# Optimization experiments

Measured on AMD Instinct MI355X. Metric: run time of the kernel, lower is better.

Reference implementation:

```python
import jax, jax.numpy as jnp
import numpy as np

B, U, V = 4, 64, 256
IN_DIM, STATE_DIM, CODE_DIM = 768, 768, 384
NUM_HEADS, HEAD_DIM = 8, 64
INNER = NUM_HEADS * HEAD_DIM  # 512
SCALE = HEAD_DIM ** 0.5


def _ln(x, g, b, eps=1e-5):
    mu = jnp.mean(x, axis=-1, keepdims=True)
    var = jnp.var(x, axis=-1, keepdims=True)
    return (x - mu) * jax.lax.rsqrt(var + eps) * g + b


def setup_inputs() -> dict:
    key = jax.random.key(0)
    ks = jax.random.split(key, 12)
    def w(k, shape, s=0.02):
        return jax.random.normal(k, shape, jnp.float32) * s
    return {
        "receiver_states": jax.random.normal(ks[0], (B, U, STATE_DIM), jnp.float32),
        "receiver_codes": jax.random.normal(ks[1], (B, U, CODE_DIM), jnp.float32),
        "sender_states": jax.random.normal(ks[2], (B, V, IN_DIM), jnp.float32),
        "ln_r_g": jnp.ones((STATE_DIM,), jnp.float32),
        "ln_r_b": jnp.zeros((STATE_DIM,), jnp.float32),
        "ln_s_g": jnp.ones((IN_DIM,), jnp.float32),
        "ln_s_b": jnp.zeros((IN_DIM,), jnp.float32),
        "Wq": w(ks[3], (STATE_DIM, INNER)), "bq": jnp.zeros((INNER,), jnp.float32), "Wmq": w(ks[4], (CODE_DIM, STATE_DIM)),
        "Wk": w(ks[5], (IN_DIM, INNER)),   "bk": jnp.zeros((INNER,), jnp.float32), "Wmk": w(ks[6], (CODE_DIM, IN_DIM)),
        "Wv": w(ks[7], (IN_DIM, INNER)),   "bv": jnp.zeros((INNER,), jnp.float32), "Wmv": w(ks[8], (CODE_DIM, IN_DIM)),
        "We": w(ks[9], (INNER, STATE_DIM)), "be": jnp.zeros((STATE_DIM,), jnp.float32), "Wme": w(ks[10], (CODE_DIM, INNER)),
        "gamma": jnp.ones((STATE_DIM,), jnp.float32),  # LayerScale, init 1.0
    }


def reference(receiver_states, receiver_codes, sender_states,
              ln_r_g, ln_r_b, ln_s_g, ln_s_b,
              Wq, bq, Wmq, Wk, bk, Wmk, Wv, bv, Wmv, We, be, Wme, gamma):
    r = _ln(receiver_states, ln_r_g, ln_r_b)   # (b,u,ds)
    s = _ln(sender_states, ln_s_g, ln_s_b)     # (b,v,di)
    # ModFC: y = (x * (1 + ctx @ Wm)) @ W + b  (code-conditioned input modulation)
    q = (r * (1.0 + receiver_codes @ Wmq)) @ Wq + bq          # (b,u,inner)
    mk = 1.0 + receiver_codes @ Wmk                           # (b,u,di)
    mv = 1.0 + receiver_codes @ Wmv                           # (b,u,di)
    xs = s[:, :, None, :]                                     # (b,v,1,di)
    k = (xs * mk[:, None, :, :]) @ Wk + bk                    # (b,v,u,inner)
    v = (xs * mv[:, None, :, :]) @ Wv + bv                    # (b,v,u,inner)
    qh = q.reshape(B, U, NUM_HEADS, HEAD_DIM)
    kh = k.reshape(B, V, U, NUM_HEADS, HEAD_DIM)
    vh = v.reshape(B, V, U, NUM_HEADS, HEAD_DIM)
    scores = jnp.einsum('buhc,bvuhc->bhuv', qh, kh) / SCALE   # (b,h,u,v)
    weights = jax.nn.softmax(scores, axis=-1)
    msg = jnp.einsum('bhuv,bvuhc->buhc', weights, vh).reshape(B, U, INNER)
    out = (msg * (1.0 + receiver_codes @ Wme)) @ We + be      # exit ModFC -> (b,u,ds)
    out = out * gamma                                         # LayerScale
    return receiver_states + out                              # residual
```

## Files before the change

kernel.cpp:

```cpp
#include <hip/hip_runtime.h>


#define DD 768
#define CDIM 384
#define NH 8
#define HD 64
#define INNER 512
#define VV 256

__device__ __forceinline__ void fma4(float4& a, float s, const float4& b) {
  a.x += s * b.x; a.y += s * b.y; a.z += s * b.z; a.w += s * b.w;
}

__device__ __forceinline__ void fma_chunk8(const float* __restrict__ Aw,
                                           int lda, int kk, const float4* b,
                                           float4* acc) {
#pragma unroll
  for (int rg = 0; rg < 4; rg++) {
    const float* ap = Aw + (rg * 2) * lda + kk;
    float4 a0l = *(const float4*)(ap);
    float4 a0h = *(const float4*)(ap + 4);
    float4 a1l = *(const float4*)(ap + lda);
    float4 a1h = *(const float4*)(ap + lda + 4);
    float4* ac = acc + rg * 2;
    fma4(ac[0], a0l.x, b[0]); fma4(ac[1], a1l.x, b[0]);
    fma4(ac[0], a0l.y, b[1]); fma4(ac[1], a1l.y, b[1]);
    fma4(ac[0], a0l.z, b[2]); fma4(ac[1], a1l.z, b[2]);
    fma4(ac[0], a0l.w, b[3]); fma4(ac[1], a1l.w, b[3]);
    fma4(ac[0], a0h.x, b[4]); fma4(ac[1], a1h.x, b[4]);
    fma4(ac[0], a0h.y, b[5]); fma4(ac[1], a1h.y, b[5]);
    fma4(ac[0], a0h.z, b[6]); fma4(ac[1], a1h.z, b[6]);
    fma4(ac[0], a0h.w, b[7]); fma4(ac[1], a1h.w, b[7]);
  }
}

template <int KQ, int NS>
__device__ __forceinline__ void gcore8(const float* __restrict__ Aw, int lda,
                                       const float* __restrict__ Bp,
                                       float4* acc) {
  float4 b0[8], b1[8];
  const float* Bq = Bp;
#pragma unroll
  for (int i = 0; i < 8; i++) b0[i] = *(const float4*)(Bq + (size_t)i * NS);
  Bq += (size_t)8 * NS;
#pragma unroll 1
  for (int kk = 0; kk + 16 <= KQ; kk += 16) {
#pragma unroll
    for (int i = 0; i < 8; i++) b1[i] = *(const float4*)(Bq + (size_t)i * NS);
    Bq += (size_t)8 * NS;
    fma_chunk8(Aw, lda, kk, b0, acc);
    if (kk + 16 < KQ) {
#pragma unroll
      for (int i = 0; i < 8; i++) b0[i] = *(const float4*)(Bq + (size_t)i * NS);
      Bq += (size_t)8 * NS;
    }
    fma_chunk8(Aw, lda, kk + 8, b1, acc);
  }
}

__device__ __forceinline__ void kred(float4* acc, float* RED, int wid,
                                     int kl) {
  __syncthreads();
  float4* R4 = (float4*)RED;
  int rg = wid & 1, kh = wid >> 1;
  if (kh) {
#pragma unroll
    for (int r = 0; r < 8; r++) R4[(rg * 8 + r) * 64 + kl] = acc[r];
  }
  __syncthreads();
  if (!kh) {
#pragma unroll
    for (int r = 0; r < 8; r++) {
      float4 v = R4[(rg * 8 + r) * 64 + kl];
      acc[r].x += v.x; acc[r].y += v.y; acc[r].z += v.z; acc[r].w += v.w;
    }
  }
}

__global__ __launch_bounds__(256, 2) void k_s1(
    const float* __restrict__ ss, const float* __restrict__ rs,
    const float* __restrict__ g_s, const float* __restrict__ b_s,
    const float* __restrict__ g_r, const float* __restrict__ b_r,
    const float* __restrict__ codes, const float* __restrict__ Wmq,
    const float* __restrict__ Wmk, const float* __restrict__ Wmv,
    const float* __restrict__ Wme, const float* __restrict__ Wk,
    float* __restrict__ s_ln, float* __restrict__ r_ln,
    float* __restrict__ cp, float* __restrict__ WkT) {
  __shared__ __align__(16) float SB[6144];
  int bid = blockIdx.x, t = threadIdx.x;
  if (bid < 176) {
    int nc = bid % 11, mb = bid / 11;
    int base = nc * 256;
    const float* W; int N, colW;
    if (base < 768)       { W = Wmq; N = DD;    colW = base; }
    else if (base < 1536) { W = Wmk; N = DD;    colW = base - 768; }
    else if (base < 2304) { W = Wmv; N = DD;    colW = base - 1536; }
    else                  { W = Wme; N = INNER; colW = base - 2304; }
    int m0 = mb * 16;
#pragma unroll
    for (int p = 0; p < 24; p++) {
      int idx = p * 256 + t, r = idx / 384, k = idx % 384;
      SB[idx] = codes[(size_t)(m0 + r) * CDIM + k];
    }
    __syncthreads();
    int kl = t & 63, wid = t >> 6, rg = wid & 1, kh = wid >> 1;
    float4 acc[8] = {};
    const float* Aw = SB + (rg * 8) * 384 + kh * 192;
    if (N == DD)
      gcore8<192, DD>(Aw, 384, W + (size_t)(kh * 192) * DD + colW + 4 * kl, acc);
    else
      gcore8<192, INNER>(Aw, 384, W + (size_t)(kh * 192) * INNER + colW + 4 * kl, acc);
    kred(acc, SB, wid, kl);
    if (!kh) {
      int gcol = base + 4 * kl;
#pragma unroll
      for (int j = 0; j < 8; j++)
        *(float4*)(cp + (size_t)(m0 + rg * 8 + j) * 2816 + gcol) = acc[j];
    }
  } else if (bid < 272) {
    int tid = bid - 176;
    int d0 = (tid >> 3) * 64, c0 = (tid & 7) * 64;
    int j = t & 63, i0 = t >> 6;
#pragma unroll
    for (int p = 0; p < 16; p++) {
      int i = p * 4 + i0;
      SB[i * 65 + j] = Wk[(size_t)(d0 + i) * INNER + c0 + j];
    }
    __syncthreads();
#pragma unroll
    for (int p = 0; p < 16; p++) {
      int i = p * 4 + i0;
      WkT[(size_t)(c0 + i) * DD + d0 + j] = SB[j * 65 + i];
    }
  } else {
    int rr = bid - 272;
    const float *x, *g, *bb; float* y; int r;
    if (rr < 1024) { x = ss; g = g_s; bb = b_s; y = s_ln; r = rr; }
    else           { x = rs; g = g_r; bb = b_r; y = r_ln; r = rr - 1024; }
    const float* xr = x + (size_t)r * DD;
    float v0 = xr[t], v1 = xr[t + 256], v2 = xr[t + 512];
    float s = v0 + v1 + v2, sq = v0 * v0 + v1 * v1 + v2 * v2;
    for (int o = 32; o > 0; o >>= 1) {
      s += __shfl_down(s, o, 64); sq += __shfl_down(sq, o, 64);
    }
    int wid = t >> 6, lane = t & 63;
    if (lane == 0) { SB[wid] = s; SB[wid + 4] = sq; }
    __syncthreads();
    float sum = SB[0] + SB[1] + SB[2] + SB[3];
    float ssq = SB[4] + SB[5] + SB[6] + SB[7];
    float mu = sum * (1.0f / 768.0f);
    float var = ssq * (1.0f / 768.0f) - mu * mu;
    float rstd = rsqrtf(var + 1e-5f);
    float* yr = y + (size_t)r * DD;
    yr[t]       = (v0 - mu) * rstd * g[t]       + bb[t];
    yr[t + 256] = (v1 - mu) * rstd * g[t + 256] + bb[t + 256];
    yr[t + 512] = (v2 - mu) * rstd * g[t + 512] + bb[t + 512];
  }
}

__global__ __launch_bounds__(256, 2) void k_s2(
    const float* __restrict__ s_ln, const float* __restrict__ r_ln,
    const float* __restrict__ cp, const float* __restrict__ Wq,
    float* __restrict__ sT, float* __restrict__ qp) {
  __shared__ __align__(16) float SB[4160];
  int bid = blockIdx.x, t = threadIdx.x;
  if (bid < 128) {
    int ks = bid & 3, tile = bid >> 2, nc = tile & 1, mb = tile >> 1;
    int m0 = mb * 16, col0 = nc * 256, k0 = ks * 192;
#pragma unroll
    for (int p = 0; p < 12; p++) {
      int idx = p * 256 + t, r = idx / 192, k = idx % 192;
      int d = k0 + k;
      float mqv = cp[(size_t)(m0 + r) * 2816 + d] + 1.0f;
      SB[idx] = r_ln[(size_t)(m0 + r) * DD + d] * mqv;
    }
    __syncthreads();
    int kl = t & 63, wid = t >> 6, rg = wid & 1, kh = wid >> 1;
    int col = col0 + 4 * kl;
    float4 acc[8] = {};
    gcore8<96, INNER>(SB + (rg * 8) * 192 + kh * 96, 192,
                      Wq + (size_t)(k0 + kh * 96) * INNER + col, acc);
    kred(acc, SB, wid, kl);
    if (!kh) {
      float* dst = qp + (size_t)ks * (256 * INNER);
#pragma unroll
      for (int j = 0; j < 8; j++)
        *(float4*)(dst + (size_t)(m0 + rg * 8 + j) * INNER + col) = acc[j];
    }
  } else {
    int tid = bid - 128;
    int vt = tid & 3, dt = (tid >> 2) % 12, b = tid / 48;
    int v0 = vt * 64, d0 = dt * 64;
    int j = t & 63, i0 = t >> 6;
#pragma unroll
    for (int p = 0; p < 16; p++) {
      int i = p * 4 + i0;
      SB[i * 65 + j] = s_ln[(size_t)(b * VV + v0 + i) * DD + d0 + j];
    }
    __syncthreads();
#pragma unroll
    for (int p = 0; p < 16; p++) {
      int i = p * 4 + i0;
      sT[((size_t)b * DD + d0 + i) * VV + v0 + j] = SB[j * 65 + i];
    }
  }
}

__global__ __launch_bounds__(256, 2) void k_s3(
    const float* __restrict__ qp, const float* __restrict__ bq,
    const float* __restrict__ WkT, const float* __restrict__ cp,
    const float* __restrict__ bk, float* __restrict__ qm,
    float* __restrict__ qbk) {
  __shared__ __align__(16) float SB[4096];
  int bid = blockIdx.x, t = threadIdx.x;
  if (bid < 384) {
    int h = bid & 7, dc = (bid >> 3) % 3, mb = bid / 24;
    int m0 = mb * 16;
#pragma unroll
    for (int p = 0; p < 4; p++) {
      int idx = p * 256 + t, r = idx >> 6, c = idx & 63;
      int i = h * HD + c;
      size_t off = (size_t)(m0 + r) * INNER + i;
      SB[idx] = qp[off] + qp[131072 + off] + qp[262144 + off] +
                qp[393216 + off] + bq[i];
    }
    __syncthreads();
    int kl = t & 63, wid = t >> 6, rg = wid & 1, kh = wid >> 1;
    int col = dc * 256 + 4 * kl;
    float4 acc[8] = {};
    gcore8<32, DD>(SB + (rg * 8) * HD + kh * 32, HD,
                   WkT + (size_t)(h * HD + kh * 32) * DD + col, acc);
    kred(acc, SB, wid, kl);
    if (!kh) {
#pragma unroll
      for (int j = 0; j < 8; j++) {
        int m = m0 + rg * 8 + j;
        const float* mkp = cp + (size_t)m * 2816 + 768 + col;
        float4 o = {acc[j].x * (mkp[0] + 1.0f), acc[j].y * (mkp[1] + 1.0f),
                    acc[j].z * (mkp[2] + 1.0f), acc[j].w * (mkp[3] + 1.0f)};
        *(float4*)(qm + ((size_t)m * NH + h) * DD + col) = o;
      }
    }
  } else {
    int m = bid - 384;
    size_t off = (size_t)m * INNER;
    SB[t] = (qp[off + t] + qp[131072 + off + t] + qp[262144 + off + t] +
             qp[393216 + off + t] + bq[t]) * bk[t];
    int t2 = t + 256;
    SB[t2] = (qp[off + t2] + qp[131072 + off + t2] + qp[262144 + off + t2] +
              qp[393216 + off + t2] + bq[t2]) * bk[t2];
    __syncthreads();
    if (t < 8) {
      float a = 0.f;
      for (int c = 0; c < HD; c++) a += SB[t * HD + c];
      qbk[m * NH + t] = a;
    }
  }
}

__global__ __launch_bounds__(256, 2) void k_s4(
    const float* __restrict__ qm, const float* __restrict__ sT,
    float* __restrict__ scp) {
  __shared__ __align__(16) float SB[4096];
  int bid = blockIdx.x, t = threadIdx.x;
  int ks = bid & 3, b = (bid >> 2) & 3, mb = bid >> 4;
  int gi0 = b * 512 + mb * 16, k0 = ks * 192;
#pragma unroll
  for (int p = 0; p < 12; p++) {
    int idx = p * 256 + t, r = idx / 192, k = idx % 192;
    SB[idx] = qm[(size_t)(gi0 + r) * DD + k0 + k];
  }
  __syncthreads();
  int kl = t & 63, wid = t >> 6, rg = wid & 1, kh = wid >> 1;
  int col = 4 * kl;
  float4 acc[8] = {};
  gcore8<96, VV>(SB + (rg * 8) * 192 + kh * 96, 192,
                 sT + ((size_t)b * DD + k0 + kh * 96) * VV + col, acc);
  kred(acc, SB, wid, kl);
  if (!kh) {
    float* dst = scp + (size_t)ks * (2048 * VV);
#pragma unroll
    for (int j = 0; j < 8; j++)
      *(float4*)(dst + (size_t)(gi0 + rg * 8 + j) * VV + col) = acc[j];
  }
}

__global__ __launch_bounds__(256, 2) void k_s5(
    const float* __restrict__ scp, const float* __restrict__ qbk,
    const float* __restrict__ s_ln, const float* __restrict__ cp,
    float* __restrict__ wsm) {
  __shared__ __align__(16) float SC[4096];
  int bid = blockIdx.x, t = threadIdx.x;
  int dc = bid % 3, up = (bid / 3) % 32, b = bid / 96;
  int gi0 = b * 512 + up * 16;
#pragma unroll
  for (int p = 0; p < 16; p++) {
    int idx = p * 256 + t, r = idx >> 8, c = idx & 255;
    size_t o = (size_t)(gi0 + r) * VV + c;
    float v = scp[o] + scp[524288 + o] + scp[1048576 + o] + scp[1572864 + o];
    int m = b * 64 + up * 2 + (r >> 3), h = r & 7;
    SC[idx] = (v + qbk[m * NH + h]) * 0.125f;
  }
  __syncthreads();
  int wid = t >> 6, lane = t & 63;
#pragma unroll
  for (int j = 0; j < 4; j++) {
    int r = wid * 4 + j;
    float x0 = SC[r * 256 + lane],       x1 = SC[r * 256 + lane + 64];
    float x2 = SC[r * 256 + lane + 128], x3 = SC[r * 256 + lane + 192];
    float mx = fmaxf(fmaxf(x0, x1), fmaxf(x2, x3));
    for (int o = 1; o < 64; o <<= 1) mx = fmaxf(mx, __shfl_xor(mx, o, 64));
    float e0 = __expf(x0 - mx), e1 = __expf(x1 - mx);
    float e2 = __expf(x2 - mx), e3 = __expf(x3 - mx);
    float sm = e0 + e1 + e2 + e3;
    for (int o = 1; o < 64; o <<= 1) sm += __shfl_xor(sm, o, 64);
    float rinv = 1.0f / sm;
    SC[r * 256 + lane] = e0 * rinv;       SC[r * 256 + lane + 64] = e1 * rinv;
    SC[r * 256 + lane + 128] = e2 * rinv; SC[r * 256 + lane + 192] = e3 * rinv;
  }
  __syncthreads();
  int kl = t & 63, rg = wid & 1, kh = wid >> 1;
  int col = dc * 256 + 4 * kl;
  float4 acc[8] = {};
  gcore8<128, DD>(SC + (rg * 8) * 256 + kh * 128, 256,
                  s_ln + (size_t)(b * VV + kh * 128) * DD + col, acc);
  kred(acc, SC, wid, kl);
  if (!kh) {
#pragma unroll
    for (int j = 0; j < 8; j++) {
      int m = b * 64 + up * 2 + rg;
      const float* mvp = cp + (size_t)m * 2816 + 1536 + col;
      float4 o = {acc[j].x * (mvp[0] + 1.0f), acc[j].y * (mvp[1] + 1.0f),
                  acc[j].z * (mvp[2] + 1.0f), acc[j].w * (mvp[3] + 1.0f)};
      *(float4*)(wsm + ((size_t)j * 256 + m) * DD + col) = o;
    }
  }
}

__global__ __launch_bounds__(256, 2) void k_s6(
    const float* __restrict__ wsm, const float* __restrict__ Wv,
    float* __restrict__ mmp) {
  __shared__ __align__(16) float AL[6144];
  int bid = blockIdx.x, t = threadIdx.x;
  int hp = bid & 1, ks = (bid >> 1) & 7, mb = bid >> 4;
  int h0 = hp * 4, m0 = mb * 16, k0 = ks * 96;
#pragma unroll
  for (int p = 0; p < 24; p++) {
    int idx = p * 256 + t;
    int e = idx / 1536, rem = idx % 1536, r = rem / 96, k = rem % 96;
    AL[idx] = wsm[((size_t)(h0 + e) * 256 + m0 + r) * DD + k0 + k];
  }
  __syncthreads();
  int kl = t & 63, wid = t >> 6, rg = wid & 1, kh = wid >> 1;
  int hs = kl >> 4, c4 = 4 * (kl & 15);
  int colg = h0 * HD + hs * HD + c4;
  const float* Aw = AL + hs * 1536 + (rg * 8) * 96 + kh * 48;
  float4 acc[8] = {};
  gcore8<48, INNER>(Aw, 96, Wv + (size_t)(k0 + kh * 48) * INNER + colg, acc);
  kred(acc, AL, wid, kl);
  if (!kh) {
    float* dst = mmp + (size_t)ks * (256 * INNER);
#pragma unroll
    for (int j = 0; j < 8; j++)
      *(float4*)(dst + (size_t)(m0 + rg * 8 + j) * INNER + colg) = acc[j];
  }
}

__global__ __launch_bounds__(256, 2) void k_s7(
    const float* __restrict__ mmp, const float* __restrict__ bvv,
    const float* __restrict__ cp, const float* __restrict__ We,
    float* __restrict__ op) {
  __shared__ __align__(16) float AL[4096];
  int bid = blockIdx.x, t = threadIdx.x;
  int ks = bid & 7, dc = (bid >> 3) % 3, mb = bid / 24;
  int m0 = mb * 16, k0 = ks * 64;
#pragma unroll
  for (int p = 0; p < 4; p++) {
    int idx = p * 256 + t, r = idx >> 6, k = idx & 63;
    int i = k0 + k;
    size_t off = (size_t)(m0 + r) * INNER + i;
    float v = mmp[off] + mmp[131072 + off] + mmp[262144 + off] +
              mmp[393216 + off] + mmp[524288 + off] + mmp[655360 + off] +
              mmp[786432 + off] + mmp[917504 + off];
    float mev = cp[(size_t)(m0 + r) * 2816 + 2304 + i] + 1.0f;
    AL[idx] = (v + bvv[i]) * mev;
  }
  __syncthreads();
  int kl = t & 63, wid = t >> 6, rg = wid & 1, kh = wid >> 1;
  int col = dc * 256 + 4 * kl;
  float4 acc[8] = {};
  gcore8<32, DD>(AL + (rg * 8) * 64 + kh * 32, 64,
                 We + (size_t)(k0 + kh * 32) * DD + col, acc);
  kred(acc, AL, wid, kl);
  if (!kh) {
    float* dst = op + (size_t)ks * (256 * DD);
#pragma unroll
    for (int j = 0; j < 8; j++)
      *(float4*)(dst + (size_t)(m0 + rg * 8 + j) * DD + col) = acc[j];
  }
}

__global__ __launch_bounds__(256) void k_s8(
    const float* __restrict__ op, const float* __restrict__ be,
    const float* __restrict__ gamma, const float* __restrict__ rs,
    float* __restrict__ outp) {
  int m = blockIdx.x, t = threadIdx.x;
#pragma unroll
  for (int j = 0; j < 3; j++) {
    int d = t + j * 256;
    size_t off = (size_t)m * DD + d;
    float v = op[off] + op[196608 + off] + op[393216 + off] +
              op[589824 + off] + op[786432 + off] + op[983040 + off] +
              op[1179648 + off] + op[1376256 + off];
    outp[off] = rs[off] + (v + be[d]) * gamma[d];
  }
}

extern "C" void kernel_launch(void* const* d_in, const int* in_sizes, int n_in,
                              void* d_out, int out_size, void* d_ws, size_t ws_size,
                              hipStream_t stream) {
  const float* rs     = (const float*)d_in[0];
  const float* codes  = (const float*)d_in[1];
  const float* ss     = (const float*)d_in[2];
  const float* ln_r_g = (const float*)d_in[3];
  const float* ln_r_b = (const float*)d_in[4];
  const float* ln_s_g = (const float*)d_in[5];
  const float* ln_s_b = (const float*)d_in[6];
  const float* Wq  = (const float*)d_in[7];
  const float* bq  = (const float*)d_in[8];
  const float* Wk  = (const float*)d_in[10];
  const float* bk  = (const float*)d_in[11];
  const float* Wmq = (const float*)d_in[9];
  const float* Wmk = (const float*)d_in[12];
  const float* Wv  = (const float*)d_in[13];
  const float* bv  = (const float*)d_in[14];
  const float* Wmv = (const float*)d_in[15];
  const float* We  = (const float*)d_in[16];
  const float* be  = (const float*)d_in[17];
  const float* Wme = (const float*)d_in[18];
  const float* gamma = (const float*)d_in[19];

  float* w = (float*)d_ws;
  float* s_ln = w;
  float* r_ln = w + 786432;
  float* WkT  = w + 983040;
  float* qp   = w + 1376256;
  float* sT   = w + 1900544;
  float* cp   = w + 2686976;
  float* qbk  = w + 3407872;
  float* qm   = w + 3409920;
  float* scp  = w + 4982784;
  float* wsm  = qm;
  float* mmp  = r_ln;
  float* op   = scp;

  k_s1<<<dim3(1552), 256, 0, stream>>>(ss, rs, ln_s_g, ln_s_b, ln_r_g, ln_r_b,
                                       codes, Wmq, Wmk, Wmv, Wme, Wk,
                                       s_ln, r_ln, cp, WkT);
  k_s2<<<dim3(320), 256, 0, stream>>>(s_ln, r_ln, cp, Wq, sT, qp);
  k_s3<<<dim3(640), 256, 0, stream>>>(qp, bq, WkT, cp, bk, qm, qbk);
  k_s4<<<dim3(512), 256, 0, stream>>>(qm, sT, scp);
  k_s5<<<dim3(384), 256, 0, stream>>>(scp, qbk, s_ln, cp, wsm);
  k_s6<<<dim3(256), 256, 0, stream>>>(wsm, Wv, mmp);
  k_s7<<<dim3(384), 256, 0, stream>>>(mmp, bv, cp, We, op);
  k_s8<<<dim3(256), 256, 0, stream>>>(op, be, gamma, rs, (float*)d_out);
}
```

Measured before the change: 186.9 us.

## Fuse final split-K reduction into atomics and vectorize partial-sum loads

Removes the separate k_s8 reduction kernel. Extra blocks in k_s6 now initialise the output with residual plus bias times gamma, and k_s7 atomically adds its gamma-scaled split-K partials straight into the output. The partial-sum staging loads in k_s3, k_s5 and k_s7 also become float4 loads. This saves one launch and the round-trip of the op buffer, at the cost of float atomics, which add contention and make the summation order nondeterministic.

```diff
diff --git a/kernel.cpp b/kernel.cpp
--- a/kernel.cpp
+++ b/kernel.cpp
@@ -8,6 +8,10 @@
 #define INNER 512
 #define VV 256
 
+__device__ __forceinline__ float4 ldf4(const float* p) {
+  return *(const float4*)(p);
+}
+
 __device__ __forceinline__ void fma4(float4& a, float s, const float4& b) {
   a.x += s * b.x; a.y += s * b.y; a.z += s * b.z; a.w += s * b.w;
 }
@@ -18,10 +22,10 @@
 #pragma unroll
   for (int rg = 0; rg < 4; rg++) {
     const float* ap = Aw + (rg * 2) * lda + kk;
-    float4 a0l = *(const float4*)(ap);
-    float4 a0h = *(const float4*)(ap + 4);
-    float4 a1l = *(const float4*)(ap + lda);
-    float4 a1h = *(const float4*)(ap + lda + 4);
+    float4 a0l = ldf4(ap);
+    float4 a0h = ldf4(ap + 4);
+    float4 a1l = ldf4(ap + lda);
+    float4 a1h = ldf4(ap + lda + 4);
     float4* ac = acc + rg * 2;
     fma4(ac[0], a0l.x, b[0]); fma4(ac[1], a1l.x, b[0]);
     fma4(ac[0], a0l.y, b[1]); fma4(ac[1], a1l.y, b[1]);
@@ -41,17 +45,17 @@
   float4 b0[8], b1[8];
   const float* Bq = Bp;
 #pragma unroll
-  for (int i = 0; i < 8; i++) b0[i] = *(const float4*)(Bq + (size_t)i * NS);
+  for (int i = 0; i < 8; i++) b0[i] = ldf4(Bq + (size_t)i * NS);
   Bq += (size_t)8 * NS;
 #pragma unroll 1
   for (int kk = 0; kk + 16 <= KQ; kk += 16) {
 #pragma unroll
-    for (int i = 0; i < 8; i++) b1[i] = *(const float4*)(Bq + (size_t)i * NS);
+    for (int i = 0; i < 8; i++) b1[i] = ldf4(Bq + (size_t)i * NS);
     Bq += (size_t)8 * NS;
     fma_chunk8(Aw, lda, kk, b0, acc);
     if (kk + 16 < KQ) {
 #pragma unroll
-      for (int i = 0; i < 8; i++) b0[i] = *(const float4*)(Bq + (size_t)i * NS);
+      for (int i = 0; i < 8; i++) b0[i] = ldf4(Bq + (size_t)i * NS);
       Bq += (size_t)8 * NS;
     }
     fma_chunk8(Aw, lda, kk + 8, b1, acc);
@@ -216,13 +220,19 @@
   if (bid < 384) {
     int h = bid & 7, dc = (bid >> 3) % 3, mb = bid / 24;
     int m0 = mb * 16;
-#pragma unroll
-    for (int p = 0; p < 4; p++) {
-      int idx = p * 256 + t, r = idx >> 6, c = idx & 63;
-      int i = h * HD + c;
+    {
+      int r = t >> 4, c4 = (t & 15) * 4;
+      int i = h * HD + c4;
       size_t off = (size_t)(m0 + r) * INNER + i;
-      SB[idx] = qp[off] + qp[131072 + off] + qp[262144 + off] +
-                qp[393216 + off] + bq[i];
+      float4 q0 = ldf4(qp + off), q1 = ldf4(qp + 131072 + off);
+      float4 q2 = ldf4(qp + 262144 + off), q3 = ldf4(qp + 393216 + off);
+      float4 bq4 = ldf4(bq + i);
+      float4 s;
+      s.x = q0.x + q1.x + q2.x + q3.x + bq4.x;
+      s.y = q0.y + q1.y + q2.y + q3.y + bq4.y;
+      s.z = q0.z + q1.z + q2.z + q3.z + bq4.z;
+      s.w = q0.w + q1.w + q2.w + q3.w + bq4.w;
+      ((float4*)SB)[t] = s;
     }
     __syncthreads();
     int kl = t & 63, wid = t >> 6, rg = wid & 1, kh = wid >> 1;
@@ -243,12 +253,18 @@
     }
   } else {
     int m = bid - 384;
-    size_t off = (size_t)m * INNER;
-    SB[t] = (qp[off + t] + qp[131072 + off + t] + qp[262144 + off + t] +
-             qp[393216 + off + t] + bq[t]) * bk[t];
-    int t2 = t + 256;
-    SB[t2] = (qp[off + t2] + qp[131072 + off + t2] + qp[262144 + off + t2] +
-              qp[393216 + off + t2] + bq[t2]) * bk[t2];
+    if (t < 128) {
+      size_t off = (size_t)m * INNER + 4 * t;
+      float4 q0 = ldf4(qp + off), q1 = ldf4(qp + 131072 + off);
+      float4 q2 = ldf4(qp + 262144 + off), q3 = ldf4(qp + 393216 + off);
+      float4 bq4 = ldf4(bq + 4 * t), bk4 = ldf4(bk + 4 * t);
+      float4 s;
+      s.x = (q0.x + q1.x + q2.x + q3.x + bq4.x) * bk4.x;
+      s.y = (q0.y + q1.y + q2.y + q3.y + bq4.y) * bk4.y;
+      s.z = (q0.z + q1.z + q2.z + q3.z + bq4.z) * bk4.z;
+      s.w = (q0.w + q1.w + q2.w + q3.w + bq4.w) * bk4.w;
+      ((float4*)SB)[t] = s;
+    }
     __syncthreads();
     if (t < 8) {
       float a = 0.f;
@@ -293,13 +309,22 @@
   int bid = blockIdx.x, t = threadIdx.x;
   int dc = bid % 3, up = (bid / 3) % 32, b = bid / 96;
   int gi0 = b * 512 + up * 16;
-#pragma unroll
-  for (int p = 0; p < 16; p++) {
-    int idx = p * 256 + t, r = idx >> 8, c = idx & 255;
-    size_t o = (size_t)(gi0 + r) * VV + c;
-    float v = scp[o] + scp[524288 + o] + scp[1048576 + o] + scp[1572864 + o];
+  float4* SC4 = (float4*)SC;
+#pragma unroll
+  for (int p = 0; p < 4; p++) {
+    int idx4 = p * 256 + t;
+    int r = idx4 >> 6, c4 = (idx4 & 63) * 4;
+    size_t o = (size_t)(gi0 + r) * VV + c4;
+    float4 v0 = ldf4(scp + o), v1 = ldf4(scp + 524288 + o);
+    float4 v2 = ldf4(scp + 1048576 + o), v3 = ldf4(scp + 1572864 + o);
     int m = b * 64 + up * 2 + (r >> 3), h = r & 7;
-    SC[idx] = (v + qbk[m * NH + h]) * 0.125f;
+    float qb = qbk[m * NH + h];
+    float4 s;
+    s.x = (v0.x + v1.x + v2.x + v3.x + qb) * 0.125f;
+    s.y = (v0.y + v1.y + v2.y + v3.y + qb) * 0.125f;
+    s.z = (v0.z + v1.z + v2.z + v3.z + qb) * 0.125f;
+    s.w = (v0.w + v1.w + v2.w + v3.w + qb) * 0.125f;
+    SC4[idx4] = s;
   }
   __syncthreads();
   int wid = t >> 6, lane = t & 63;
@@ -339,51 +364,75 @@
 
 __global__ __launch_bounds__(256, 2) void k_s6(
     const float* __restrict__ wsm, const float* __restrict__ Wv,
-    float* __restrict__ mmp) {
+    float* __restrict__ mmp, const float* __restrict__ rs,
+    const float* __restrict__ be, const float* __restrict__ gamma,
+    float* __restrict__ outp) {
   __shared__ __align__(16) float AL[6144];
   int bid = blockIdx.x, t = threadIdx.x;
-  int hp = bid & 1, ks = (bid >> 1) & 7, mb = bid >> 4;
-  int h0 = hp * 4, m0 = mb * 16, k0 = ks * 96;
-#pragma unroll
-  for (int p = 0; p < 24; p++) {
-    int idx = p * 256 + t;
-    int e = idx / 1536, rem = idx % 1536, r = rem / 96, k = rem % 96;
-    AL[idx] = wsm[((size_t)(h0 + e) * 256 + m0 + r) * DD + k0 + k];
-  }
-  __syncthreads();
-  int kl = t & 63, wid = t >> 6, rg = wid & 1, kh = wid >> 1;
-  int hs = kl >> 4, c4 = 4 * (kl & 15);
-  int colg = h0 * HD + hs * HD + c4;
-  const float* Aw = AL + hs * 1536 + (rg * 8) * 96 + kh * 48;
-  float4 acc[8] = {};
-  gcore8<48, INNER>(Aw, 96, Wv + (size_t)(k0 + kh * 48) * INNER + colg, acc);
-  kred(acc, AL, wid, kl);
-  if (!kh) {
-    float* dst = mmp + (size_t)ks * (256 * INNER);
-#pragma unroll
-    for (int j = 0; j < 8; j++)
-      *(float4*)(dst + (size_t)(m0 + rg * 8 + j) * INNER + colg) = acc[j];
+  if (bid < 256) {
+    int hp = bid & 1, ks = (bid >> 1) & 7, mb = bid >> 4;
+    int h0 = hp * 4, m0 = mb * 16, k0 = ks * 96;
+#pragma unroll
+    for (int p = 0; p < 24; p++) {
+      int idx = p * 256 + t;
+      int e = idx / 1536, rem = idx % 1536, r = rem / 96, k = rem % 96;
+      AL[idx] = wsm[((size_t)(h0 + e) * 256 + m0 + r) * DD + k0 + k];
+    }
+    __syncthreads();
+    int kl = t & 63, wid = t >> 6, rg = wid & 1, kh = wid >> 1;
+    int hs = kl >> 4, c4 = 4 * (kl & 15);
+    int colg = h0 * HD + hs * HD + c4;
+    const float* Aw = AL + hs * 1536 + (rg * 8) * 96 + kh * 48;
+    float4 acc[8] = {};
+    gcore8<48, INNER>(Aw, 96, Wv + (size_t)(k0 + kh * 48) * INNER + colg, acc);
+    kred(acc, AL, wid, kl);
+    if (!kh) {
+      float* dst = mmp + (size_t)ks * (256 * INNER);
+#pragma unroll
+      for (int j = 0; j < 8; j++)
+        *(float4*)(dst + (size_t)(m0 + rg * 8 + j) * INNER + colg) = acc[j];
+    }
+  } else {
+    int ib = bid - 256;
+#pragma unroll
+    for (int p = 0; p < 8; p++) {
+      int i4 = ib * 2048 + p * 256 + t;
+      int d = (i4 % 192) * 4;
+      float4 rv = ldf4(rs + (size_t)i4 * 4);
+      float4 bev = ldf4(be + d), gv = ldf4(gamma + d);
+      float4 o = {rv.x + bev.x * gv.x, rv.y + bev.y * gv.y,
+                  rv.z + bev.z * gv.z, rv.w + bev.w * gv.w};
+      *(float4*)(outp + (size_t)i4 * 4) = o;
+    }
   }
 }
 
 __global__ __launch_bounds__(256, 2) void k_s7(
     const float* __restrict__ mmp, const float* __restrict__ bvv,
     const float* __restrict__ cp, const float* __restrict__ We,
-    float* __restrict__ op) {
+    const float* __restrict__ gamma, float* __restrict__ outp) {
   __shared__ __align__(16) float AL[4096];
   int bid = blockIdx.x, t = threadIdx.x;
   int ks = bid & 7, dc = (bid >> 3) % 3, mb = bid / 24;
   int m0 = mb * 16, k0 = ks * 64;
-#pragma unroll
-  for (int p = 0; p < 4; p++) {
-    int idx = p * 256 + t, r = idx >> 6, k = idx & 63;
-    int i = k0 + k;
+  {
+    int r = t >> 4, k4 = (t & 15) * 4;
+    int i = k0 + k4;
     size_t off = (size_t)(m0 + r) * INNER + i;
-    float v = mmp[off] + mmp[131072 + off] + mmp[262144 + off] +
-              mmp[393216 + off] + mmp[524288 + off] + mmp[655360 + off] +
-              mmp[786432 + off] + mmp[917504 + off];
-    float mev = cp[(size_t)(m0 + r) * 2816 + 2304 + i] + 1.0f;
-    AL[idx] = (v + bvv[i]) * mev;
+    float4 v = ldf4(mmp + off);
+    float4 m1 = ldf4(mmp + 131072 + off), m2 = ldf4(mmp + 262144 + off);
+    float4 m3 = ldf4(mmp + 393216 + off), m4 = ldf4(mmp + 524288 + off);
+    float4 m5 = ldf4(mmp + 655360 + off), m6 = ldf4(mmp + 786432 + off);
+    float4 m7 = ldf4(mmp + 917504 + off);
+    v.x = v.x + m1.x + m2.x + m3.x + m4.x + m5.x + m6.x + m7.x;
+    v.y = v.y + m1.y + m2.y + m3.y + m4.y + m5.y + m6.y + m7.y;
+    v.z = v.z + m1.z + m2.z + m3.z + m4.z + m5.z + m6.z + m7.z;
+    v.w = v.w + m1.w + m2.w + m3.w + m4.w + m5.w + m6.w + m7.w;
+    float4 me = ldf4(cp + (size_t)(m0 + r) * 2816 + 2304 + i);
+    float4 bv4 = ldf4(bvv + i);
+    float4 res = {(v.x + bv4.x) * (me.x + 1.0f), (v.y + bv4.y) * (me.y + 1.0f),
+                  (v.z + bv4.z) * (me.z + 1.0f), (v.w + bv4.w) * (me.w + 1.0f)};
+    ((float4*)AL)[t] = res;
   }
   __syncthreads();
   int kl = t & 63, wid = t >> 6, rg = wid & 1, kh = wid >> 1;
@@ -393,26 +442,15 @@
                  We + (size_t)(k0 + kh * 32) * DD + col, acc);
   kred(acc, AL, wid, kl);
   if (!kh) {
-    float* dst = op + (size_t)ks * (256 * DD);
-#pragma unroll
-    for (int j = 0; j < 8; j++)
-      *(float4*)(dst + (size_t)(m0 + rg * 8 + j) * DD + col) = acc[j];
-  }
-}
-
-__global__ __launch_bounds__(256) void k_s8(
-    const float* __restrict__ op, const float* __restrict__ be,
-    const float* __restrict__ gamma, const float* __restrict__ rs,
-    float* __restrict__ outp) {
-  int m = blockIdx.x, t = threadIdx.x;
-#pragma unroll
-  for (int j = 0; j < 3; j++) {
-    int d = t + j * 256;
-    size_t off = (size_t)m * DD + d;
-    float v = op[off] + op[196608 + off] + op[393216 + off] +
-              op[589824 + off] + op[786432 + off] + op[983040 + off] +
-              op[1179648 + off] + op[1376256 + off];
-    outp[off] = rs[off] + (v + be[d]) * gamma[d];
+    float4 gv = ldf4(gamma + col);
+#pragma unroll
+    for (int j = 0; j < 8; j++) {
+      float* dst = outp + (size_t)(m0 + rg * 8 + j) * DD + col;
+      unsafeAtomicAdd(dst + 0, acc[j].x * gv.x);
+      unsafeAtomicAdd(dst + 1, acc[j].y * gv.y);
+      unsafeAtomicAdd(dst + 2, acc[j].z * gv.z);
+      unsafeAtomicAdd(dst + 3, acc[j].w * gv.w);
+    }
   }
 }
 
@@ -452,7 +490,6 @@
   float* scp  = w + 4982784;
   float* wsm  = qm;
   float* mmp  = r_ln;
-  float* op   = scp;
 
   k_s1<<<dim3(1552), 256, 0, stream>>>(ss, rs, ln_s_g, ln_s_b, ln_r_g, ln_r_b,
                                        codes, Wmq, Wmk, Wmv, Wme, Wk,
@@ -461,7 +498,7 @@
   k_s3<<<dim3(640), 256, 0, stream>>>(qp, bq, WkT, cp, bk, qm, qbk);
   k_s4<<<dim3(512), 256, 0, stream>>>(qm, sT, scp);
   k_s5<<<dim3(384), 256, 0, stream>>>(scp, qbk, s_ln, cp, wsm);
-  k_s6<<<dim3(256), 256, 0, stream>>>(wsm, Wv, mmp);
-  k_s7<<<dim3(384), 256, 0, stream>>>(mmp, bv, cp, We, op);
-  k_s8<<<dim3(256), 256, 0, stream>>>(op, be, gamma, rs, (float*)d_out);
-}
+  k_s6<<<dim3(280), 256, 0, stream>>>(wsm, Wv, mmp, rs, be, gamma,
+                                      (float*)d_out);
+  k_s7<<<dim3(384), 256, 0, stream>>>(mmp, bv, cp, We, gamma, (float*)d_out);
+}
```

Result: slower. 196.0 us (+4.9%).
